# Kernel optimization log

Hardware: AMD Instinct MI355X
Metric: run time of the kernel (lower is better)

The kernel has to match this reference:

```python
import jax, jax.numpy as jnp
import numpy as np

WH, WW = 7, 7
N_TOK = WH * WW


def _buffers():
    # relative_coords_table: [1, 2*WH-1, 2*WW-1, 2], Swin-V2 log-spaced coords
    ch = np.arange(-(WH - 1), WH, dtype=np.float32)
    cw = np.arange(-(WW - 1), WW, dtype=np.float32)
    t = np.stack(np.meshgrid(ch, cw, indexing='ij'), axis=-1)[None]
    t[..., 0] /= (WH - 1)
    t[..., 1] /= (WW - 1)
    t *= 8.0
    t = np.sign(t) * np.log2(np.abs(t) + 1.0) / np.log2(8.0)
    # relative_position_index: [N, N]
    coords = np.stack(np.meshgrid(np.arange(WH), np.arange(WW), indexing='ij'))
    cf = coords.reshape(2, -1)
    rc = (cf[:, :, None] - cf[:, None, :]).transpose(1, 2, 0).astype(np.int32)
    rc[..., 0] += WH - 1
    rc[..., 1] += WW - 1
    rc[..., 0] *= 2 * WW - 1
    idx = rc.sum(-1)
    return jnp.asarray(t, jnp.float32), jnp.asarray(idx, jnp.int32)


def setup_inputs() -> dict:
    key = jax.random.key(0)
    ks = jax.random.split(key, 10)
    C, H = 384, 12
    B_, nW = 2048, 64
    rel_table, rel_index = _buffers()
    s = 0.02
    return {
        'x': jax.random.normal(ks[0], (B_, N_TOK, C), jnp.float32),
        'mask': jax.random.normal(ks[1], (nW, N_TOK, N_TOK), jnp.float32),
        'qkv_w': jax.random.normal(ks[2], (3 * C, C), jnp.float32) * s,
        'q_bias': jnp.zeros((C,), jnp.float32),
        'v_bias': jnp.zeros((C,), jnp.float32),
        'logit_scale': jnp.full((H, 1, 1), np.log(10.0), jnp.float32),
        'cpb_w1': jax.random.normal(ks[3], (512, 2), jnp.float32) * s,
        'cpb_b1': jnp.zeros((512,), jnp.float32),
        'cpb_w2': jax.random.normal(ks[4], (H, 512), jnp.float32) * s,
        'proj_w': jax.random.normal(ks[5], (C, C), jnp.float32) * s,
        'proj_b': jnp.zeros((C,), jnp.float32),
        'rel_table': rel_table,
        'rel_index': rel_index,
    }


def reference(x, mask, qkv_w, q_bias, v_bias, logit_scale, cpb_w1, cpb_b1,
              cpb_w2, proj_w, proj_b, rel_table, rel_index):
    B_, N, C = x.shape
    H = logit_scale.shape[0]
    Dh = C // H
    nW = mask.shape[0]
    # qkv projection with q/v bias, zero bias for k
    qkv_bias = jnp.concatenate([q_bias, jnp.zeros_like(v_bias), v_bias])
    qkv = x @ qkv_w.T + qkv_bias                       # [B, N, 3C]
    qkv = qkv.reshape(B_, N, 3, H, Dh).transpose(2, 0, 3, 1, 4)
    q, k, v = qkv[0], qkv[1], qkv[2]                    # [B, H, N, Dh]
    # per-head clamped logit scale
    ls = jnp.exp(jnp.minimum(logit_scale, np.log(1.0 / 0.01)))  # [H,1,1]
    # continuous relative position bias via small MLP
    tbl = jax.nn.relu(rel_table @ cpb_w1.T + cpb_b1) @ cpb_w2.T  # [1,13,13,H]
    tbl = tbl.reshape(-1, H)
    rpb = tbl[rel_index.reshape(-1)].reshape(N, N, H).transpose(2, 0, 1)
    rpb = 16.0 * jax.nn.sigmoid(rpb)                    # [H, N, N]
    # cosine attention (kernel uses norm + 1e-6 in denominator)
    qn = q / (jnp.sqrt(jnp.sum(q * q, -1, keepdims=True)) + 1e-6)
    kn = k / (jnp.sqrt(jnp.sum(k * k, -1, keepdims=True)) + 1e-6)
    attn = jnp.einsum('bhnd,bhmd->bhnm', qn, kn) * ls[None]
    attn = attn + rpb[None]
    # shift mask: window index w = batch_index % nW
    attn = attn.reshape(B_ // nW, nW, H, N, N) + mask[None, :, None]
    attn = attn.reshape(B_, H, N, N)
    # stable softmax with kernel's +1e-6 in denominator
    m = jnp.max(attn, -1, keepdims=True)
    e = jnp.exp(attn - m)
    p = e / (jnp.sum(e, -1, keepdims=True) + 1e-6)
    out = jnp.einsum('bhnm,bhmd->bhnd', p, v)           # [B, H, N, Dh]
    out = out.transpose(0, 2, 1, 3).reshape(B_, N, C)
    return out @ proj_w.T + proj_b
```

## Files before the change

kernel.cpp:

```cpp
#include <hip/hip_runtime.h>
#include <hip/hip_bf16.h>

typedef __attribute__((ext_vector_type(8))) short bf16x8;
typedef __attribute__((ext_vector_type(4))) float f32x4;
typedef __attribute__((ext_vector_type(16))) float f32x16;
typedef __attribute__((ext_vector_type(8))) unsigned short u16x8;
typedef unsigned short ushort_t;

#define DEVFN static __device__ __forceinline__

DEVFN ushort_t f2bf(float f) {
  unsigned int u = __builtin_bit_cast(unsigned int, f);
  u += 0x7FFFu + ((u >> 16) & 1u);
  return (ushort_t)(u >> 16);
}

DEVFN unsigned int cvtpk_bf16(float lo, float hi) {
  unsigned int r;
  asm("v_cvt_pk_bf16_f32 %0, %1, %2" : "=v"(r) : "v"(lo), "v"(hi));
  return r;
}

DEVFN void gload_lds16(const void* g, void* l) {
  __builtin_amdgcn_global_load_lds(
      (const __attribute__((address_space(1))) void*)g,
      (__attribute__((address_space(3))) void*)l, 16, 0, 0);
}

DEVFN int xcd_swz(int bid, int nwg) {
  int q = nwg >> 3, r = nwg & 7;
  int xcd = bid & 7, u = bid >> 3;
  return (xcd < r ? xcd * (q + 1) : r * (q + 1) + (xcd - r) * q) + u;
}

__global__ void k_prep_w(const float* __restrict__ qkv_w, const float* __restrict__ proj_w,
                         const float* __restrict__ q_bias, const float* __restrict__ v_bias,
                         ushort_t* __restrict__ qkv_wb, ushort_t* __restrict__ proj_wb,
                         float* __restrict__ qkv_bias) {
  int gid = blockIdx.x * blockDim.x + threadIdx.x;
  int stride = gridDim.x * blockDim.x;
  for (int i = gid; i < 1152 * 384; i += stride) qkv_wb[i] = f2bf(qkv_w[i]);
  for (int i = gid; i < 384 * 384; i += stride) proj_wb[i] = f2bf(proj_w[i]);
  for (int i = gid; i < 1152; i += stride)
    qkv_bias[i] = (i < 384) ? q_bias[i] : ((i < 768) ? 0.f : v_bias[i - 768]);
}

__global__ void k_xb(const float* __restrict__ x, ushort_t* __restrict__ xb, long n4) {
  long gid = (long)blockIdx.x * blockDim.x + threadIdx.x;
  long stride = (long)gridDim.x * blockDim.x;
  for (long i = gid; i < n4; i += stride) {
    float4 v = reinterpret_cast<const float4*>(x)[i];
    unsigned long long pk = (unsigned long long)f2bf(v.x) |
                            ((unsigned long long)f2bf(v.y) << 16) |
                            ((unsigned long long)f2bf(v.z) << 32) |
                            ((unsigned long long)f2bf(v.w) << 48);
    reinterpret_cast<unsigned long long*>(xb)[i] = pk;
  }
}

__global__ void k_prep_cpb(const float* __restrict__ rel_table, const float* __restrict__ cpb_w1,
                           const float* __restrict__ cpb_b1, const float* __restrict__ cpb_w2,
                           const float* __restrict__ logit_scale,
                           float* __restrict__ tbl, float* __restrict__ ls) {
  int lane = threadIdx.x;
  if (blockIdx.x == 169) {
    if (lane < 12) ls[lane] = __expf(fminf(logit_scale[lane], 4.605170185988092f));
    return;
  }
  int row = blockIdx.x;
  float t0 = rel_table[row * 2 + 0], t1 = rel_table[row * 2 + 1];
  float acc[12];
#pragma unroll
  for (int h = 0; h < 12; h++) acc[h] = 0.f;
  for (int j = lane; j < 512; j += 64) {
    float hj = fmaxf(cpb_w1[j * 2] * t0 + cpb_w1[j * 2 + 1] * t1 + cpb_b1[j], 0.f);
#pragma unroll
    for (int h = 0; h < 12; h++) acc[h] += cpb_w2[h * 512 + j] * hj;
  }
#pragma unroll
  for (int h = 0; h < 12; h++) {
    float v = acc[h];
    v += __shfl_xor(v, 1);  v += __shfl_xor(v, 2);  v += __shfl_xor(v, 4);
    v += __shfl_xor(v, 8);  v += __shfl_xor(v, 16); v += __shfl_xor(v, 32);
    if (lane == 0) tbl[row * 12 + h] = v;
  }
}

__global__ void k_prep_comb(const float* __restrict__ tbl, const int* __restrict__ rel_index,
                            const float* __restrict__ mask, float* __restrict__ comb) {
  int gid = blockIdx.x * blockDim.x + threadIdx.x;
  if (gid >= 64 * 12 * 2401) return;
  int ij = gid % 2401;
  int h = (gid / 2401) % 12;
  int w = gid / (2401 * 12);
  float t = tbl[rel_index[ij] * 12 + h];
  comb[(size_t)(w * 12 + h) * 2404 + ij] = 16.f / (1.f + __expf(-t)) + mask[w * 2401 + ij];
}

__global__ void __launch_bounds__(512, 4) k_qkv(const ushort_t* __restrict__ xb,
                                                const ushort_t* __restrict__ wb,
                                                const float* __restrict__ bias,
                                                const float* __restrict__ lsb,
                                                ushort_t* __restrict__ qkvn, int nmb) {
  __shared__ __align__(16) ushort_t As[256][64];
  __shared__ __align__(16) ushort_t Bs[128][64];
  const int tid = threadIdx.x;
  const int lane = tid & 63, wid = tid >> 6;
  const int wm = wid >> 1, wn = wid & 1;
  const int l15 = lane & 15, g = lane >> 4;
  const int t = xcd_swz(blockIdx.x, nmb * 9);
  const int m0 = (t / 9) * 256, n0 = (t % 9) * 128;
  f32x4 acc[4][4] = {};

  const int rb_ = (wid << 3) + (lane >> 3);
  const int cg_ = (lane & 7) ^ (rb_ & 7);
  const size_t so_ = (size_t)rb_ * 384 + cg_ * 8;
  const int lo_ = wid * 512;

#define QKV_STAGE(kk)                                                        \
  {                                                                          \
    const ushort_t* ga = xb + (size_t)m0 * 384 + (kk) * 64;                  \
    const ushort_t* gb = wb + (size_t)n0 * 384 + (kk) * 64;                  \
    _Pragma("unroll")                                                        \
    for (int it = 0; it < 4; it++)                                           \
      gload_lds16(ga + so_ + (size_t)it * 24576, &As[0][0] + lo_ + it * 4096);\
    _Pragma("unroll")                                                        \
    for (int it = 0; it < 2; it++)                                           \
      gload_lds16(gb + so_ + (size_t)it * 24576, &Bs[0][0] + lo_ + it * 4096);\
  }

  for (int kk = 0; kk < 6; kk++) {
    __syncthreads();
    QKV_STAGE(kk);
    __syncthreads();
#pragma unroll
    for (int ks = 0; ks < 64; ks += 32) {
      const int cxor = (ks >> 3) + g;
      bf16x8 a[4], b[4];
#pragma unroll
      for (int mi = 0; mi < 4; mi++) {
        int row = wm * 64 + mi * 16 + l15;
        a[mi] = *reinterpret_cast<const bf16x8*>(&As[row][(cxor ^ (row & 7)) * 8]);
      }
#pragma unroll
      for (int ni = 0; ni < 4; ni++) {
        int row = wn * 64 + ni * 16 + l15;
        b[ni] = *reinterpret_cast<const bf16x8*>(&Bs[row][(cxor ^ (row & 7)) * 8]);
      }
#pragma unroll
      for (int mi = 0; mi < 4; mi++)
#pragma unroll
        for (int ni = 0; ni < 4; ni++)
          acc[mi][ni] = __builtin_amdgcn_mfma_f32_16x16x32_bf16(a[mi], b[ni], acc[mi][ni], 0, 0, 0);
    }
  }
#undef QKV_STAGE
  const int colbase = n0 + wn * 64;
  const int which = colbase / 384;
  const float scl0 = (which == 0) ? lsb[(colbase >> 5)] : 1.f;
  const float scl1 = (which == 0) ? lsb[(colbase >> 5) + 1] : 1.f;
  float bs[4];
#pragma unroll
  for (int ni = 0; ni < 4; ni++) bs[ni] = bias[colbase + ni * 16 + l15];
#pragma unroll
  for (int mi = 0; mi < 4; mi++) {
#pragma unroll
    for (int r = 0; r < 4; r++) {
      float v[4];
#pragma unroll
      for (int ni = 0; ni < 4; ni++) v[ni] = acc[mi][ni][r] + bs[ni];
      if (which < 2) {
        float ss0 = v[0] * v[0] + v[1] * v[1];
        float ss1 = v[2] * v[2] + v[3] * v[3];
        ss0 += __shfl_xor(ss0, 1); ss1 += __shfl_xor(ss1, 1);
        ss0 += __shfl_xor(ss0, 2); ss1 += __shfl_xor(ss1, 2);
        ss0 += __shfl_xor(ss0, 4); ss1 += __shfl_xor(ss1, 4);
        ss0 += __shfl_xor(ss0, 8); ss1 += __shfl_xor(ss1, 8);
        float rn0 = scl0 / (sqrtf(ss0) + 1e-6f);
        float rn1 = scl1 / (sqrtf(ss1) + 1e-6f);
        v[0] *= rn0; v[1] *= rn0; v[2] *= rn1; v[3] *= rn1;
      }
      int row = m0 + wm * 64 + mi * 16 + g * 4 + r;
      size_t base = (size_t)row * 1152 + colbase + l15;
#pragma unroll
      for (int ni = 0; ni < 4; ni++) qkvn[base + ni * 16] = f2bf(v[ni]);
    }
  }
}

__global__ void __launch_bounds__(256, 4) k_attn(const ushort_t* __restrict__ qkvn,
                                                 const float* __restrict__ comb,
                                                 ushort_t* __restrict__ attn,
                                                 int win_base, int nk) {
  __shared__ __align__(16) float comb_s[50][52];
  __shared__ __align__(16) ushort_t Vt[4][32][72];
  const int tid = threadIdx.x;
  const int lane = tid & 63, wv = tid >> 6;
  const int l31 = lane & 31, hi = lane >> 5;
  const int h = blockIdx.y;
  const int wloc = blockIdx.x & 63;
  const int k = (blockIdx.x >> 6) * 4 + wv;
  const bool active = k < nk;
  const int w_abs = (win_base + wloc) & 63;
  const size_t rowbase = (size_t)(wloc + 64 * k) * 49;

  u16x8 vreg[4];
  bf16x8 qf[2][2], kf[2][2];
  if (active) {
#pragma unroll
    for (int pass = 0; pass < 4; pass++) {
      int t = pass * 16 + (lane >> 2);
      int d0 = (lane & 3) * 8;
      u16x8 v = {};
      if (t < 49)
        v = *reinterpret_cast<const u16x8*>(&qkvn[(rowbase + t) * 1152 + 768 + h * 32 + d0]);
      vreg[pass] = v;
    }
#pragma unroll
    for (int b = 0; b < 2; b++) {
      int t = b * 32 + l31; if (t > 48) t = 48;
      size_t rb = (rowbase + t) * 1152 + h * 32 + hi * 8;
#pragma unroll
      for (int ks = 0; ks < 2; ks++) {
        qf[b][ks] = *reinterpret_cast<const bf16x8*>(&qkvn[rb + ks * 16]);
        kf[b][ks] = *reinterpret_cast<const bf16x8*>(&qkvn[rb + 384 + ks * 16]);
      }
    }
  }

  {
    const float* ct = comb + (size_t)(w_abs * 12 + h) * 2404;
    for (int i4 = tid; i4 < 600; i4 += 256) {
      float4 v = *reinterpret_cast<const float4*>(&ct[i4 * 4]);
      int e = i4 * 4;
      comb_s[(e + 0) / 49][(e + 0) % 49] = v.x;
      comb_s[(e + 1) / 49][(e + 1) % 49] = v.y;
      comb_s[(e + 2) / 49][(e + 2) % 49] = v.z;
      comb_s[(e + 3) / 49][(e + 3) % 49] = v.w;
    }
    if (tid == 0) comb_s[48][48] = ct[2400];
  }
  if (active) {
#pragma unroll
    for (int pass = 0; pass < 4; pass++) {
      int t = pass * 16 + (lane >> 2);
      int d0 = (lane & 3) * 8;
#pragma unroll
      for (int j = 0; j < 8; j++) Vt[wv][d0 + j][t] = vreg[pass][j];
    }
  }
  __syncthreads();
  if (!active) return;

  f32x16 S[2][2] = {};
#pragma unroll
  for (int a = 0; a < 2; a++)
#pragma unroll
    for (int b = 0; b < 2; b++) {
      S[a][b] = __builtin_amdgcn_mfma_f32_32x32x16_bf16(kf[a][0], qf[b][0], S[a][b], 0, 0, 0);
      S[a][b] = __builtin_amdgcn_mfma_f32_32x32x16_bf16(kf[a][1], qf[b][1], S[a][b], 0, 0, 0);
    }

#pragma unroll
  for (int b = 0; b < 2; b++) {
    const int qt = b * 32 + l31;
    const bool qok = qt < 49;
    const int qi = qok ? qt : 48;
    float m = -3.0e38f;
#pragma unroll
    for (int a = 0; a < 2; a++)
#pragma unroll
      for (int rq = 0; rq < 4; rq++) {
        f32x4 ch = *reinterpret_cast<const f32x4*>(&comb_s[qi][a * 32 + rq * 8 + hi * 4]);
#pragma unroll
        for (int j = 0; j < 4; j++) {
          int r = rq * 4 + j;
          int kt = a * 32 + rq * 8 + hi * 4 + j;
          float v = (qok && kt < 49) ? (S[a][b][r] + ch[j]) : -3.0e38f;
          S[a][b][r] = v;
          m = fmaxf(m, v);
        }
      }
    m = fmaxf(m, __shfl_xor(m, 32));
    float s = 0.f;
#pragma unroll
    for (int a = 0; a < 2; a++)
#pragma unroll
      for (int r = 0; r < 16; r++) {
        float e = __expf(S[a][b][r] - m);
        S[a][b][r] = e;
        s += e;
      }
    s += __shfl_xor(s, 32);
    const float inv = 1.f / (s + 1e-6f);
    unsigned int pkk[2][4][2];
#pragma unroll
    for (int a = 0; a < 2; a++)
#pragma unroll
      for (int c = 0; c < 4; c++) {
        pkk[a][c][0] = cvtpk_bf16(S[a][b][c * 4 + 0] * inv, S[a][b][c * 4 + 1] * inv);
        pkk[a][c][1] = cvtpk_bf16(S[a][b][c * 4 + 2] * inv, S[a][b][c * 4 + 3] * inv);
      }
    f32x16 O = {};
#pragma unroll
    for (int a = 0; a < 2; a++)
#pragma unroll
      for (int ks = 0; ks < 2; ks++) {
        unsigned int s0 = hi ? pkk[a][2 * ks][0] : pkk[a][2 * ks + 1][0];
        unsigned int s1 = hi ? pkk[a][2 * ks][1] : pkk[a][2 * ks + 1][1];
        unsigned int r0 = __shfl_xor(s0, 32);
        unsigned int r1 = __shfl_xor(s1, 32);
        unsigned int w0 = hi ? r0 : pkk[a][2 * ks][0];
        unsigned int w1 = hi ? r1 : pkk[a][2 * ks][1];
        unsigned int w2 = hi ? pkk[a][2 * ks + 1][0] : r0;
        unsigned int w3 = hi ? pkk[a][2 * ks + 1][1] : r1;
        uint4 wq = {w0, w1, w2, w3};
        bf16x8 pa = __builtin_bit_cast(bf16x8, wq);
        bf16x8 vb = *reinterpret_cast<const bf16x8*>(&Vt[wv][l31][a * 32 + ks * 16 + hi * 8]);
        O = __builtin_amdgcn_mfma_f32_32x32x16_bf16(pa, vb, O, 0, 0, 0);
      }
#pragma unroll
    for (int r = 0; r < 16; r++) {
      int qrow = b * 32 + (r & 3) + 8 * (r >> 2) + 4 * hi;
      if (qrow < 49)
        attn[(rowbase + qrow) * 384 + h * 32 + l31] = f2bf(O[r]);
    }
  }
}

__global__ void __launch_bounds__(512, 4) k_proj(const ushort_t* __restrict__ a,
                                                 const ushort_t* __restrict__ wb,
                                                 const float* __restrict__ pbias,
                                                 float* __restrict__ out, int nmb) {
  __shared__ __align__(16) ushort_t As[256][64];
  __shared__ __align__(16) ushort_t Bs[128][64];
  const int tid = threadIdx.x;
  const int lane = tid & 63, wid = tid >> 6;
  const int wm = wid >> 1, wn = wid & 1;
  const int l15 = lane & 15, g = lane >> 4;
  const int t = xcd_swz(blockIdx.x, nmb * 3);
  const int m0 = (t / 3) * 256, n0 = (t % 3) * 128;
  f32x4 acc[4][4] = {};

  const int rb_ = (wid << 3) + (lane >> 3);
  const int cg_ = (lane & 7) ^ (rb_ & 7);
  const size_t so_ = (size_t)rb_ * 384 + cg_ * 8;
  const int lo_ = wid * 512;

#define PRJ_STAGE(kk)                                                        \
  {                                                                          \
    const ushort_t* ga = a + (size_t)m0 * 384 + (kk) * 64;                   \
    const ushort_t* gb = wb + (size_t)n0 * 384 + (kk) * 64;                  \
    _Pragma("unroll")                                                        \
    for (int it = 0; it < 4; it++)                                           \
      gload_lds16(ga + so_ + (size_t)it * 24576, &As[0][0] + lo_ + it * 4096);\
    _Pragma("unroll")                                                        \
    for (int it = 0; it < 2; it++)                                           \
      gload_lds16(gb + so_ + (size_t)it * 24576, &Bs[0][0] + lo_ + it * 4096);\
  }

  for (int kk = 0; kk < 6; kk++) {
    __syncthreads();
    PRJ_STAGE(kk);
    __syncthreads();
#pragma unroll
    for (int ks = 0; ks < 64; ks += 32) {
      const int cxor = (ks >> 3) + g;
      bf16x8 av[4], bv[4];
#pragma unroll
      for (int mi = 0; mi < 4; mi++) {
        int row = wm * 64 + mi * 16 + l15;
        av[mi] = *reinterpret_cast<const bf16x8*>(&As[row][(cxor ^ (row & 7)) * 8]);
      }
#pragma unroll
      for (int ni = 0; ni < 4; ni++) {
        int row = wn * 64 + ni * 16 + l15;
        bv[ni] = *reinterpret_cast<const bf16x8*>(&Bs[row][(cxor ^ (row & 7)) * 8]);
      }
#pragma unroll
      for (int mi = 0; mi < 4; mi++)
#pragma unroll
        for (int ni = 0; ni < 4; ni++)
          acc[mi][ni] = __builtin_amdgcn_mfma_f32_16x16x32_bf16(av[mi], bv[ni], acc[mi][ni], 0, 0, 0);
    }
  }
#undef PRJ_STAGE
  const int colbase = n0 + wn * 64;
  float bs[4];
#pragma unroll
  for (int ni = 0; ni < 4; ni++) bs[ni] = pbias[colbase + ni * 16 + l15];
#pragma unroll
  for (int mi = 0; mi < 4; mi++)
#pragma unroll
    for (int r = 0; r < 4; r++) {
      int row = m0 + wm * 64 + mi * 16 + g * 4 + r;
#pragma unroll
      for (int ni = 0; ni < 4; ni++)
        out[(size_t)row * 384 + colbase + ni * 16 + l15] = acc[mi][ni][r] + bs[ni];
    }
}

extern "C" void kernel_launch(void* const* d_in, const int* in_sizes, int n_in,
                              void* d_out, int out_size, void* d_ws, size_t ws_size,
                              hipStream_t stream) {
  const float* x        = (const float*)d_in[0];
  const float* mask     = (const float*)d_in[1];
  const float* qkv_w    = (const float*)d_in[2];
  const float* q_bias   = (const float*)d_in[3];
  const float* v_bias   = (const float*)d_in[4];
  const float* logit_sc = (const float*)d_in[5];
  const float* cpb_w1   = (const float*)d_in[6];
  const float* cpb_b1   = (const float*)d_in[7];
  const float* cpb_w2   = (const float*)d_in[8];
  const float* proj_w   = (const float*)d_in[9];
  const float* proj_b   = (const float*)d_in[10];
  const float* rel_tab  = (const float*)d_in[11];
  const int*   rel_idx  = (const int*)d_in[12];
  float* out = (float*)d_out;

  char* p = (char*)d_ws;
  auto carve = [&](size_t bytes) { char* r = p; p += (bytes + 255) & ~(size_t)255; return r; };
  ushort_t* qkv_wb  = (ushort_t*)carve(1152 * 384 * 2);
  ushort_t* proj_wb = (ushort_t*)carve(384 * 384 * 2);
  float* qkv_bias   = (float*)carve(1152 * 4);
  float* tbl        = (float*)carve(169 * 12 * 4);
  float* lsb        = (float*)carve(12 * 4);
  float* comb       = (float*)carve((size_t)64 * 12 * 2404 * 4);
  size_t fixed = (size_t)(p - (char*)d_ws);
  size_t avail = ws_size > fixed ? ws_size - fixed : 0;

  int nc = 1;
  while (nc < 8) {
    size_t per = ((size_t)(2048 / nc)) * 49 * (384 + 1152 + 384) * 2 + (1 << 20);
    if (per <= avail) break;
    nc *= 2;
  }
  const int nwin = 2048 / nc;
  const size_t Mc = (size_t)nwin * 49;
  ushort_t* xbuf  = (ushort_t*)carve(Mc * 384 * 2);
  ushort_t* qkvn  = (ushort_t*)carve(Mc * 1152 * 2);
  ushort_t* attnb = (ushort_t*)carve(Mc * 384 * 2);
  const int nmb = (int)(Mc / 256);
  const int nk = nwin >> 6;

  k_prep_w<<<dim3(512), dim3(256), 0, stream>>>(qkv_w, proj_w, q_bias, v_bias, qkv_wb, proj_wb, qkv_bias);
  k_prep_cpb<<<dim3(170), dim3(64), 0, stream>>>(rel_tab, cpb_w1, cpb_b1, cpb_w2, logit_sc, tbl, lsb);
  k_prep_comb<<<dim3((64 * 12 * 2401 + 255) / 256), dim3(256), 0, stream>>>(tbl, rel_idx, mask, comb);

  for (int c = 0; c < nc; c++) {
    size_t roff = (size_t)c * Mc;
    k_xb<<<dim3(2048), dim3(256), 0, stream>>>(x + roff * 384, xbuf, (long)(Mc * 384 / 4));
    k_qkv<<<dim3(nmb * 9), dim3(512), 0, stream>>>(xbuf, qkv_wb, qkv_bias, lsb, qkvn, nmb);
    k_attn<<<dim3(64 * ((nk + 3) / 4), 12), dim3(256), 0, stream>>>(qkvn, comb, attnb, c * nwin, nk);
    k_proj<<<dim3(nmb * 3), dim3(512), 0, stream>>>(attnb, proj_wb, proj_b, out + roff * 384, nmb);
  }
}
```

Baseline: 388.9 us.

## Retile QKV and proj GEMMs to 128x384 tiles with 2x4 warp grid

Both GEMM kernels change from 256x128 to 128x384 output tiles. Each of the 8 waves now computes a 64x96 subtile, and the proj kernel covers the full 384 output columns per block. A/B staging loads and launch grids are adjusted to match, and the chunk-count loop bound is raised. The intent is to read the A operand (activations) only once per row block across all N columns, cutting redundant global traffic. In exchange the kernels use more accumulator registers and launch bounds drop to 2 blocks per CU, which may lower occupancy.

```diff
diff --git a/kernel.cpp b/kernel.cpp
--- a/kernel.cpp
+++ b/kernel.cpp
@@ -97,23 +97,23 @@
   comb[(size_t)(w * 12 + h) * 2404 + ij] = 16.f / (1.f + __expf(-t)) + mask[w * 2401 + ij];
 }
 
-__global__ void __launch_bounds__(512, 4) k_qkv(const ushort_t* __restrict__ xb,
+__global__ void __launch_bounds__(512, 2) k_qkv(const ushort_t* __restrict__ xb,
                                                 const ushort_t* __restrict__ wb,
                                                 const float* __restrict__ bias,
                                                 const float* __restrict__ lsb,
                                                 ushort_t* __restrict__ qkvn, int nmb) {
-  __shared__ __align__(16) ushort_t As[256][64];
-  __shared__ __align__(16) ushort_t Bs[128][64];
+  __shared__ __align__(16) ushort_t As[128][64];
+  __shared__ __align__(16) ushort_t Bs[384][64];
   const int tid = threadIdx.x;
   const int lane = tid & 63, wid = tid >> 6;
-  const int wm = wid >> 1, wn = wid & 1;
+  const int wm = wid >> 2, wn = wid & 3;
   const int l15 = lane & 15, g = lane >> 4;
-  const int t = xcd_swz(blockIdx.x, nmb * 9);
-  const int m0 = (t / 9) * 256, n0 = (t % 9) * 128;
-  f32x4 acc[4][4] = {};
-
-  const int rb_ = (wid << 3) + (lane >> 3);
-  const int cg_ = (lane & 7) ^ (rb_ & 7);
+  const int t = xcd_swz(blockIdx.x, nmb * 3);
+  const int m0 = (t / 3) * 128, n0 = (t % 3) * 384;
+  f32x4 acc[4][6] = {};
+
+  const int rb_ = tid >> 3;
+  const int cg_ = (tid & 7) ^ (rb_ & 7);
   const size_t so_ = (size_t)rb_ * 384 + cg_ * 8;
   const int lo_ = wid * 512;
 
@@ -122,10 +122,10 @@
     const ushort_t* ga = xb + (size_t)m0 * 384 + (kk) * 64;                  \
     const ushort_t* gb = wb + (size_t)n0 * 384 + (kk) * 64;                  \
     _Pragma("unroll")                                                        \
-    for (int it = 0; it < 4; it++)                                           \
+    for (int it = 0; it < 2; it++)                                           \
       gload_lds16(ga + so_ + (size_t)it * 24576, &As[0][0] + lo_ + it * 4096);\
     _Pragma("unroll")                                                        \
-    for (int it = 0; it < 2; it++)                                           \
+    for (int it = 0; it < 6; it++)                                           \
       gload_lds16(gb + so_ + (size_t)it * 24576, &Bs[0][0] + lo_ + it * 4096);\
   }
 
@@ -136,54 +136,57 @@
 #pragma unroll
     for (int ks = 0; ks < 64; ks += 32) {
       const int cxor = (ks >> 3) + g;
-      bf16x8 a[4], b[4];
+      bf16x8 a[4], b[6];
 #pragma unroll
       for (int mi = 0; mi < 4; mi++) {
         int row = wm * 64 + mi * 16 + l15;
         a[mi] = *reinterpret_cast<const bf16x8*>(&As[row][(cxor ^ (row & 7)) * 8]);
       }
 #pragma unroll
-      for (int ni = 0; ni < 4; ni++) {
-        int row = wn * 64 + ni * 16 + l15;
+      for (int ni = 0; ni < 6; ni++) {
+        int row = wn * 96 + ni * 16 + l15;
         b[ni] = *reinterpret_cast<const bf16x8*>(&Bs[row][(cxor ^ (row & 7)) * 8]);
       }
 #pragma unroll
       for (int mi = 0; mi < 4; mi++)
 #pragma unroll
-        for (int ni = 0; ni < 4; ni++)
+        for (int ni = 0; ni < 6; ni++)
           acc[mi][ni] = __builtin_amdgcn_mfma_f32_16x16x32_bf16(a[mi], b[ni], acc[mi][ni], 0, 0, 0);
     }
   }
 #undef QKV_STAGE
-  const int colbase = n0 + wn * 64;
-  const int which = colbase / 384;
-  const float scl0 = (which == 0) ? lsb[(colbase >> 5)] : 1.f;
-  const float scl1 = (which == 0) ? lsb[(colbase >> 5) + 1] : 1.f;
-  float bs[4];
-#pragma unroll
-  for (int ni = 0; ni < 4; ni++) bs[ni] = bias[colbase + ni * 16 + l15];
+  const int colbase = n0 + wn * 96;
+  const int which = n0 / 384;
+  float scl[3];
+#pragma unroll
+  for (int p = 0; p < 3; p++)
+    scl[p] = (which == 0) ? lsb[(colbase >> 5) + p] : 1.f;
+  float bs[6];
+#pragma unroll
+  for (int ni = 0; ni < 6; ni++) bs[ni] = bias[colbase + ni * 16 + l15];
 #pragma unroll
   for (int mi = 0; mi < 4; mi++) {
 #pragma unroll
     for (int r = 0; r < 4; r++) {
-      float v[4];
-#pragma unroll
-      for (int ni = 0; ni < 4; ni++) v[ni] = acc[mi][ni][r] + bs[ni];
+      float v[6];
+#pragma unroll
+      for (int ni = 0; ni < 6; ni++) v[ni] = acc[mi][ni][r] + bs[ni];
       if (which < 2) {
-        float ss0 = v[0] * v[0] + v[1] * v[1];
-        float ss1 = v[2] * v[2] + v[3] * v[3];
-        ss0 += __shfl_xor(ss0, 1); ss1 += __shfl_xor(ss1, 1);
-        ss0 += __shfl_xor(ss0, 2); ss1 += __shfl_xor(ss1, 2);
-        ss0 += __shfl_xor(ss0, 4); ss1 += __shfl_xor(ss1, 4);
-        ss0 += __shfl_xor(ss0, 8); ss1 += __shfl_xor(ss1, 8);
-        float rn0 = scl0 / (sqrtf(ss0) + 1e-6f);
-        float rn1 = scl1 / (sqrtf(ss1) + 1e-6f);
-        v[0] *= rn0; v[1] *= rn0; v[2] *= rn1; v[3] *= rn1;
+#pragma unroll
+        for (int p = 0; p < 3; p++) {
+          float ss = v[2 * p] * v[2 * p] + v[2 * p + 1] * v[2 * p + 1];
+          ss += __shfl_xor(ss, 1);
+          ss += __shfl_xor(ss, 2);
+          ss += __shfl_xor(ss, 4);
+          ss += __shfl_xor(ss, 8);
+          float rn = scl[p] / (sqrtf(ss) + 1e-6f);
+          v[2 * p] *= rn; v[2 * p + 1] *= rn;
+        }
       }
       int row = m0 + wm * 64 + mi * 16 + g * 4 + r;
       size_t base = (size_t)row * 1152 + colbase + l15;
 #pragma unroll
-      for (int ni = 0; ni < 4; ni++) qkvn[base + ni * 16] = f2bf(v[ni]);
+      for (int ni = 0; ni < 6; ni++) qkvn[base + ni * 16] = f2bf(v[ni]);
     }
   }
 }
@@ -328,34 +331,34 @@
   }
 }
 
-__global__ void __launch_bounds__(512, 4) k_proj(const ushort_t* __restrict__ a,
+__global__ void __launch_bounds__(512, 2) k_proj(const ushort_t* __restrict__ a,
                                                  const ushort_t* __restrict__ wb,
                                                  const float* __restrict__ pbias,
                                                  float* __restrict__ out, int nmb) {
-  __shared__ __align__(16) ushort_t As[256][64];
-  __shared__ __align__(16) ushort_t Bs[128][64];
+  __shared__ __align__(16) ushort_t As[128][64];
+  __shared__ __align__(16) ushort_t Bs[384][64];
   const int tid = threadIdx.x;
   const int lane = tid & 63, wid = tid >> 6;
-  const int wm = wid >> 1, wn = wid & 1;
+  const int wm = wid >> 2, wn = wid & 3;
   const int l15 = lane & 15, g = lane >> 4;
-  const int t = xcd_swz(blockIdx.x, nmb * 3);
-  const int m0 = (t / 3) * 256, n0 = (t % 3) * 128;
-  f32x4 acc[4][4] = {};
-
-  const int rb_ = (wid << 3) + (lane >> 3);
-  const int cg_ = (lane & 7) ^ (rb_ & 7);
+  const int t = xcd_swz(blockIdx.x, nmb);
+  const int m0 = t * 128;
+  f32x4 acc[4][6] = {};
+
+  const int rb_ = tid >> 3;
+  const int cg_ = (tid & 7) ^ (rb_ & 7);
   const size_t so_ = (size_t)rb_ * 384 + cg_ * 8;
   const int lo_ = wid * 512;
 
 #define PRJ_STAGE(kk)                                                        \
   {                                                                          \
     const ushort_t* ga = a + (size_t)m0 * 384 + (kk) * 64;                   \
-    const ushort_t* gb = wb + (size_t)n0 * 384 + (kk) * 64;                  \
+    const ushort_t* gb = wb + (size_t)(kk) * 64;                             \
     _Pragma("unroll")                                                        \
-    for (int it = 0; it < 4; it++)                                           \
+    for (int it = 0; it < 2; it++)                                           \
       gload_lds16(ga + so_ + (size_t)it * 24576, &As[0][0] + lo_ + it * 4096);\
     _Pragma("unroll")                                                        \
-    for (int it = 0; it < 2; it++)                                           \
+    for (int it = 0; it < 6; it++)                                           \
       gload_lds16(gb + so_ + (size_t)it * 24576, &Bs[0][0] + lo_ + it * 4096);\
   }
 
@@ -366,36 +369,36 @@
 #pragma unroll
     for (int ks = 0; ks < 64; ks += 32) {
       const int cxor = (ks >> 3) + g;
-      bf16x8 av[4], bv[4];
+      bf16x8 av[4], bv[6];
 #pragma unroll
       for (int mi = 0; mi < 4; mi++) {
         int row = wm * 64 + mi * 16 + l15;
         av[mi] = *reinterpret_cast<const bf16x8*>(&As[row][(cxor ^ (row & 7)) * 8]);
       }
 #pragma unroll
-      for (int ni = 0; ni < 4; ni++) {
-        int row = wn * 64 + ni * 16 + l15;
+      for (int ni = 0; ni < 6; ni++) {
+        int row = wn * 96 + ni * 16 + l15;
         bv[ni] = *reinterpret_cast<const bf16x8*>(&Bs[row][(cxor ^ (row & 7)) * 8]);
       }
 #pragma unroll
       for (int mi = 0; mi < 4; mi++)
 #pragma unroll
-        for (int ni = 0; ni < 4; ni++)
+        for (int ni = 0; ni < 6; ni++)
           acc[mi][ni] = __builtin_amdgcn_mfma_f32_16x16x32_bf16(av[mi], bv[ni], acc[mi][ni], 0, 0, 0);
     }
   }
 #undef PRJ_STAGE
-  const int colbase = n0 + wn * 64;
-  float bs[4];
-#pragma unroll
-  for (int ni = 0; ni < 4; ni++) bs[ni] = pbias[colbase + ni * 16 + l15];
+  const int colbase = wn * 96;
+  float bs[6];
+#pragma unroll
+  for (int ni = 0; ni < 6; ni++) bs[ni] = pbias[colbase + ni * 16 + l15];
 #pragma unroll
   for (int mi = 0; mi < 4; mi++)
 #pragma unroll
     for (int r = 0; r < 4; r++) {
       int row = m0 + wm * 64 + mi * 16 + g * 4 + r;
 #pragma unroll
-      for (int ni = 0; ni < 4; ni++)
+      for (int ni = 0; ni < 6; ni++)
         out[(size_t)row * 384 + colbase + ni * 16 + l15] = acc[mi][ni][r] + bs[ni];
     }
 }
@@ -430,7 +433,7 @@
   size_t avail = ws_size > fixed ? ws_size - fixed : 0;
 
   int nc = 1;
-  while (nc < 8) {
+  while (nc < 16) {
     size_t per = ((size_t)(2048 / nc)) * 49 * (384 + 1152 + 384) * 2 + (1 << 20);
     if (per <= avail) break;
     nc *= 2;
@@ -440,7 +443,7 @@
   ushort_t* xbuf  = (ushort_t*)carve(Mc * 384 * 2);
   ushort_t* qkvn  = (ushort_t*)carve(Mc * 1152 * 2);
   ushort_t* attnb = (ushort_t*)carve(Mc * 384 * 2);
-  const int nmb = (int)(Mc / 256);
+  const int nmb = (int)(Mc / 128);
   const int nk = nwin >> 6;
 
   k_prep_w<<<dim3(512), dim3(256), 0, stream>>>(qkv_w, proj_w, q_bias, v_bias, qkv_wb, proj_wb, qkv_bias);
@@ -450,8 +453,8 @@
   for (int c = 0; c < nc; c++) {
     size_t roff = (size_t)c * Mc;
     k_xb<<<dim3(2048), dim3(256), 0, stream>>>(x + roff * 384, xbuf, (long)(Mc * 384 / 4));
-    k_qkv<<<dim3(nmb * 9), dim3(512), 0, stream>>>(xbuf, qkv_wb, qkv_bias, lsb, qkvn, nmb);
+    k_qkv<<<dim3(nmb * 3), dim3(512), 0, stream>>>(xbuf, qkv_wb, qkv_bias, lsb, qkvn, nmb);
     k_attn<<<dim3(64 * ((nk + 3) / 4), 12), dim3(256), 0, stream>>>(qkvn, comb, attnb, c * nwin, nk);
-    k_proj<<<dim3(nmb * 3), dim3(512), 0, stream>>>(attnb, proj_wb, proj_b, out + roff * 384, nmb);
-  }
-}
+    k_proj<<<dim3(nmb), dim3(512), 0, stream>>>(attnb, proj_wb, proj_b, out + roff * 384, nmb);
+  }
+}
```

Result: slower. 444.7 us (+14.4%).
